# Kernel tuning notes

Hardware: AMD Instinct MI355X
Metric: run time of the kernel (lower is better)

Reference implementation:

```python
import jax, jax.numpy as jnp
import numpy as np

MUL = 256            # multiplicity of each irrep block
S = MUL              # scalar (0e) block width
V = MUL * 3          # vector (1e) block width
D = S + V            # total feature width = 1024
N = 32768            # number of nodes
INV3 = 1.0 / np.sqrt(3.0)   # w3j(1,1,0) and w3j(0,1,1) coefficient
INV6 = 1.0 / np.sqrt(6.0)   # w3j(1,1,1) (Levi-Civita) coefficient
A0 = np.sqrt(1.0 / 5.0)     # path weight for 0e outputs: sqrt(dim_out / n_paths) = sqrt(1/5)
A1 = np.sqrt(3.0 / 5.0)     # path weight for 1e outputs: sqrt(3/5)


def _split(x):
    # x: [N, D] -> scalars [N, MUL], vectors [N, MUL, 3]
    return x[:, :S], x[:, S:].reshape(x.shape[0], MUL, 3)


def norm_gate(x, w1, b1, w2, b2):
    # NormGate: gates = MLP([scalars, |vectors|]); out = [gates_s, vectors * gates_v]
    s, v = _split(x)
    nv = jnp.sqrt(jnp.sum(v * v, axis=-1) + 1e-12)           # [N, MUL] per-irrep norms
    f0 = jnp.concatenate([s, nv], axis=-1)                    # [N, 2*MUL]
    g = jax.nn.silu(f0 @ w1 + b1) @ w2 + b2                   # [N, 2*MUL]
    gated = v * g[:, S:, None]                                # ElementwiseTensorProduct with 0e gates
    return jnp.concatenate([g[:, :S], gated.reshape(-1, V)], axis=-1)


def irrep_linear(x, w0, b0, w1):
    # e3nn o3.Linear: per-l multiplicity mixing with 1/sqrt(fan_in) normalization; bias only on 0e
    s, v = _split(x)
    so = s @ (w0 / np.sqrt(MUL)) + b0
    vo = jnp.einsum('nui,uw->nwi', v, w1 / np.sqrt(MUL))
    return jnp.concatenate([so, vo.reshape(-1, V)], axis=-1)


def tensor_product(x1, x2, w):
    # 'uuu' CG tensor product, 5 instructions: (0,0)->0, (0,1)->1, (1,0)->1, (1,1)->0, (1,1)->1
    # w: [5, MUL] per-path per-u learned weights
    s1, v1 = _split(x1)
    s2, v2 = _split(x2)
    out0 = A0 * (w[0] * s1 * s2 + w[3] * INV3 * jnp.sum(v1 * v2, axis=-1))   # [N, MUL]
    out1 = A1 * (INV3 * (w[1] * s1)[:, :, None] * v2
                 + INV3 * (w[2] * s2)[:, :, None] * v1
                 + INV6 * w[4][None, :, None] * jnp.cross(v1, v2))           # [N, MUL, 3]
    return jnp.concatenate([out0, out1.reshape(-1, V)], axis=-1)


def setup_inputs() -> dict:
    key = jax.random.key(0)
    ks = jax.random.split(key, 32)
    d = {}
    d['x'] = jax.random.normal(ks[0], (N, D), dtype=jnp.float32)
    d['old_fii'] = jax.random.normal(ks[1], (N, D), dtype=jnp.float32)
    i = 2
    for pre in ('ng1', 'ng2', 'ngo'):
        d[pre + '_w1'] = jax.random.normal(ks[i], (2 * MUL, 2 * MUL), dtype=jnp.float32) / np.sqrt(2 * MUL); i += 1
        d[pre + '_b1'] = jax.random.normal(ks[i], (2 * MUL,), dtype=jnp.float32) * 0.01; i += 1
        d[pre + '_w2'] = jax.random.normal(ks[i], (2 * MUL, 2 * MUL), dtype=jnp.float32) / np.sqrt(2 * MUL); i += 1
        d[pre + '_b2'] = jax.random.normal(ks[i], (2 * MUL,), dtype=jnp.float32) * 0.01; i += 1
    for pre in ('lin1', 'lin2', 'lin3'):
        d[pre + '_w0'] = jax.random.normal(ks[i], (MUL, MUL), dtype=jnp.float32); i += 1
        d[pre + '_b0'] = jax.random.normal(ks[i], (MUL,), dtype=jnp.float32) * 0.01; i += 1
        d[pre + '_w1'] = jax.random.normal(ks[i], (MUL, MUL), dtype=jnp.float32); i += 1
    d['tp_w'] = jax.random.normal(ks[i], (5, MUL), dtype=jnp.float32)
    return d


def reference(x, old_fii,
              ng1_w1, ng1_b1, ng1_w2, ng1_b2,
              ng2_w1, ng2_b1, ng2_w2, ng2_b2,
              ngo_w1, ngo_b1, ngo_w2, ngo_b2,
              lin1_w0, lin1_b0, lin1_w1,
              lin2_w0, lin2_b0, lin2_w1,
              lin3_w0, lin3_b0, lin3_w1,
              tp_w):
    xl = irrep_linear(norm_gate(x, ng1_w1, ng1_b1, ng1_w2, ng1_b2), lin1_w0, lin1_b0, lin1_w1)
    xr = irrep_linear(norm_gate(x, ng2_w1, ng2_b1, ng2_w2, ng2_b2), lin2_w0, lin2_b0, lin2_w1)
    t = tensor_product(xl, xr, tp_w) + x        # resnet (dims match)
    t = irrep_linear(norm_gate(t, ngo_w1, ngo_b1, ngo_w2, ngo_b2), lin3_w0, lin3_b0, lin3_w1)
    return old_fii + t
```

## Files before the change

kernel.cpp:

```cpp
#include <hip/hip_runtime.h>
#include <stdint.h>
#include <math.h>

typedef unsigned short u16;
typedef __attribute__((ext_vector_type(8))) short short8;
typedef __attribute__((ext_vector_type(4))) float f32x4;

#define A0C 0.44721359549995793f
#define A1C 0.77459666924148340f
#define INV3C 0.57735026918962584f
#define INV6C 0.40824829046386302f

__device__ __forceinline__ float bf2f(u16 u) {
    unsigned v = ((unsigned)u) << 16; float f; __builtin_memcpy(&f, &v, 4); return f;
}
__device__ __forceinline__ u16 f2bf(float f) {
    unsigned u; __builtin_memcpy(&u, &f, 4);
    u += 0x7fffu + ((u >> 16) & 1u);
    return (u16)(u >> 16);
}

__device__ __forceinline__ void gload_lds16(const void* g, void* l) {
    __builtin_amdgcn_global_load_lds((const __attribute__((address_space(1))) unsigned*)g,
                                     (__attribute__((address_space(3))) unsigned*)l, 16, 0, 0);
}

union S8 { short8 v; u16 h[8]; };

struct WDesc { const float* s; u16* d; int n; float sc; };
struct WArgs { WDesc w[12]; };

__global__ void cvt_weights(WArgs args) {
    WDesc wd = args.w[blockIdx.z];
    int n = wd.n;
    int x0 = blockIdx.x * 32, y0 = blockIdx.y * 32;
    if (x0 >= n || y0 >= n) return;
    __shared__ float tile[32][33];
    int tx = threadIdx.x, ty = threadIdx.y;
#pragma unroll
    for (int j = 0; j < 4; j++)
        tile[ty + 8 * j][tx] = wd.s[(size_t)(y0 + ty + 8 * j) * n + x0 + tx];
    __syncthreads();
#pragma unroll
    for (int j = 0; j < 4; j++)
        wd.d[(size_t)(x0 + ty + 8 * j) * n + y0 + tx] = f2bf(tile[tx][ty + 8 * j] * wd.sc);
}

struct BDesc { const float* s; float* d; int n; };
struct BArgs { BDesc b[9]; };
__global__ void pack_bias(BArgs a) {
    BDesc b = a.b[blockIdx.x];
    for (int i = threadIdx.x; i < b.n; i += 256) b.d[i] = b.s[i];
}

__global__ void prep_f0(const float* __restrict__ x, u16* __restrict__ f0,
                        u16* __restrict__ xv, long ps) {
    int t = blockIdx.x * 256 + threadIdx.x;
    long n = t >> 5;
    int u0 = (t & 31) * 8;
    const float* xr = x + (size_t)n * 1024;
    float4 s0 = *(const float4*)(xr + u0);
    float4 s1 = *(const float4*)(xr + u0 + 4);
    float vv[24];
#pragma unroll
    for (int i = 0; i < 6; i++) {
        float4 w = *(const float4*)(xr + 256 + 3 * u0 + 4 * i);
        vv[4 * i] = w.x; vv[4 * i + 1] = w.y; vv[4 * i + 2] = w.z; vv[4 * i + 3] = w.w;
    }
    float sc[8] = { s0.x, s0.y, s0.z, s0.w, s1.x, s1.y, s1.z, s1.w };
    S8 fs, fn, px, py, pz;
#pragma unroll
    for (int j = 0; j < 8; j++) {
        float a = vv[3 * j], b = vv[3 * j + 1], c = vv[3 * j + 2];
        float nv = sqrtf(a * a + b * b + c * c + 1e-12f);
        fs.h[j] = f2bf(sc[j]);
        fn.h[j] = f2bf(nv);
        px.h[j] = f2bf(a); py.h[j] = f2bf(b); pz.h[j] = f2bf(c);
    }
    size_t o = (size_t)n * 256 + u0;
    *(short8*)(f0 + (size_t)n * 512 + u0) = fs.v;
    *(short8*)(f0 + (size_t)n * 512 + 256 + u0) = fn.v;
    *(short8*)(xv + o) = px.v;
    *(short8*)(xv + ps + o) = py.v;
    *(short8*)(xv + 2 * ps + o) = pz.v;
}

__global__ __launch_bounds__(512, 2)
void gemm256(const u16* __restrict__ Ap, int lda, long az,
             const u16* __restrict__ xsrc,
             const u16* __restrict__ gp, int gld, long gz,
             const u16* __restrict__ Bt, long bz, long bw,
             const float* __restrict__ bias, int bsz,
             u16* __restrict__ C, int ldc, long czs, long czp,
             int K, long nc, int mode, int act, int nshift)
{
    extern __shared__ __align__(16) u16 sm[];
    u16* As = sm;
    u16* Bs = sm + 32768;

    const int tid = threadIdx.x;
    const int lane = tid & 63;
    const int wid = tid >> 6;
    const int wr = wid >> 2, wc = wid & 3;
    const int lr = lane & 15, hk = lane >> 4;

    int nwg = gridDim.x;
    int lid = blockIdx.x;
    int wg;
    if ((nwg & 7) == 0) { int q = nwg >> 3; wg = (lid & 7) * q + (lid >> 3); }
    else wg = lid;
    const long row0 = (long)(wg >> nshift) * 256;
    const int n0 = (wg & ((1 << nshift) - 1)) * 256;
    const int zi = blockIdx.y;

    long p = 0, rr0 = row0;
    if (mode == 2) { p = row0 / nc; rr0 = row0 - p * nc; }

    const u16* Bz = Bt + (size_t)zi * bz + ((mode == 2 && p > 0) ? bw : 0);
    const long cbase = (mode == 2) ? (zi * czs + p * czp + rr0 * ldc)
                                   : (zi * czs + row0 * ldc);

    f32x4 acc[8][4];
#pragma unroll
    for (int m = 0; m < 8; m++)
#pragma unroll
        for (int n = 0; n < 4; n++) acc[m][n] = (f32x4){0.f, 0.f, 0.f, 0.f};

    auto stageB = [&](int buf, int kt) {
#pragma unroll
        for (int it = 0; it < 4; ++it) {
            int idx = it * 512 + tid;
            int r = idx >> 3, s = idx & 7;
            const u16* g = Bz + (size_t)(n0 + r) * K + kt + ((s ^ (r & 7)) * 8);
            u16* l = Bs + buf * 16384 + (size_t)(it * 512 + (tid & 0x1C0)) * 8;
            gload_lds16(g, l);
        }
    };
    auto stageA0 = [&](int buf, int kt) {
#pragma unroll
        for (int it = 0; it < 4; ++it) {
            int idx = it * 512 + tid;
            int r = idx >> 3, s = idx & 7;
            const u16* g = Ap + (size_t)zi * az + (rr0 + r) * (size_t)lda + kt + ((s ^ (r & 7)) * 8);
            u16* l = As + buf * 16384 + (size_t)(it * 512 + (tid & 0x1C0)) * 8;
            gload_lds16(g, l);
        }
    };
    auto stageA2 = [&](int buf, int kt) {
#pragma unroll
        for (int it = 0; it < 4; ++it) {
            int idx = it * 512 + tid;
            int r = idx >> 3, s = idx & 7;
            int u = kt + s * 8;
            S8 gg, tu, pk;
            gg.v = *(const short8*)(gp + (size_t)zi * gz + (rr0 + r) * (size_t)gld + 256 + u);
            tu.v = *(const short8*)(xsrc + (size_t)(row0 - nc + r) * 256 + u);
#pragma unroll
            for (int j = 0; j < 8; j++) pk.h[j] = f2bf(bf2f(tu.h[j]) * bf2f(gg.h[j]));
            *(short8*)&As[buf * 16384 + ((size_t)r * 8 + (s ^ (r & 7))) * 8] = pk.v;
        }
    };

    const bool a_direct = (mode == 0) || (p == 0);
    const int nt = K >> 6;
    stageB(0, 0);
    if (a_direct) stageA0(0, 0); else stageA2(0, 0);
    __syncthreads();

    int buf = 0;
    for (int t = 0; t < nt; ++t) {
        if (t + 1 < nt) {
            int kt = (t + 1) << 6;
            stageB(buf ^ 1, kt);
            if (a_direct) stageA0(buf ^ 1, kt); else stageA2(buf ^ 1, kt);
        }
        const int ao = buf * 16384, bo = buf * 16384;
#pragma unroll
        for (int kk = 0; kk < 2; ++kk) {
            short8 b[4];
#pragma unroll
            for (int n = 0; n < 4; n++) {
                int cb = wc * 64 + n * 16 + lr;
                int sl = (kk * 4 + hk) ^ (cb & 7);
                b[n] = *(const short8*)&Bs[bo + (size_t)cb * 64 + sl * 8];
            }
#pragma unroll
            for (int m = 0; m < 8; m++) {
                int ra = wr * 128 + m * 16 + lr;
                int sl = (kk * 4 + hk) ^ (ra & 7);
                short8 a = *(const short8*)&As[ao + (size_t)ra * 64 + sl * 8];
#pragma unroll
                for (int n = 0; n < 4; n++)
                    acc[m][n] = __builtin_amdgcn_mfma_f32_16x16x32_bf16(b[n], a, acc[m][n], 0, 0, 0);
            }
        }
        __syncthreads();
        buf ^= 1;
    }

    const bool use_bias = bias && (mode == 0 || p == 0);
#pragma unroll
    for (int m = 0; m < 8; m++) {
        long rit = wr * 128 + m * 16 + lr;
        u16* crow = C + cbase + rit * (size_t)ldc;
#pragma unroll
        for (int n = 0; n < 4; n++) {
            int col = n0 + wc * 64 + n * 16 + hk * 4;
            float4 bb = use_bias ? *(const float4*)&bias[(size_t)zi * bsz + col]
                                 : (float4){0.f, 0.f, 0.f, 0.f};
            float v0 = acc[m][n][0] + bb.x;
            float v1 = acc[m][n][1] + bb.y;
            float v2 = acc[m][n][2] + bb.z;
            float v3 = acc[m][n][3] + bb.w;
            if (act) {
                v0 = v0 * (1.0f / (1.0f + __expf(-v0)));
                v1 = v1 * (1.0f / (1.0f + __expf(-v1)));
                v2 = v2 * (1.0f / (1.0f + __expf(-v2)));
                v3 = v3 * (1.0f / (1.0f + __expf(-v3)));
            }
            uint2 st;
            st.x = (unsigned)f2bf(v0) | ((unsigned)f2bf(v1) << 16);
            st.y = (unsigned)f2bf(v2) | ((unsigned)f2bf(v3) << 16);
            *(uint2*)(crow + col) = st;
        }
    }
}

__global__ void tp_res(const u16* __restrict__ xl, const u16* xr_,
                       const float* __restrict__ tpw, const u16* __restrict__ xv,
                       u16* f0, u16* tv, long ps)
{
    int t = blockIdx.x * 256 + threadIdx.x;
    long n = t >> 5;
    int u0 = (t & 31) * 8;
    size_t o = (size_t)n * 256 + u0;

    S8 S1, AX, AY, AZ, S2, BX, BY, BZ, XS, RX, RY, RZ;
    S1.v = *(const short8*)(xl + o);
    AX.v = *(const short8*)(xl + ps + o);
    AY.v = *(const short8*)(xl + 2 * ps + o);
    AZ.v = *(const short8*)(xl + 3 * ps + o);
    S2.v = *(const short8*)(xr_ + o);
    BX.v = *(const short8*)(xr_ + ps + o);
    BY.v = *(const short8*)(xr_ + 2 * ps + o);
    BZ.v = *(const short8*)(xr_ + 3 * ps + o);
    XS.v = *(const short8*)(f0 + (size_t)n * 512 + u0);
    RX.v = *(const short8*)(xv + o);
    RY.v = *(const short8*)(xv + ps + o);
    RZ.v = *(const short8*)(xv + 2 * ps + o);

    float W[5][8];
#pragma unroll
    for (int q = 0; q < 5; q++) {
        float4 a = *(const float4*)(tpw + q * 256 + u0);
        float4 b = *(const float4*)(tpw + q * 256 + u0 + 4);
        W[q][0] = a.x; W[q][1] = a.y; W[q][2] = a.z; W[q][3] = a.w;
        W[q][4] = b.x; W[q][5] = b.y; W[q][6] = b.z; W[q][7] = b.w;
    }

    S8 O0, NV, TX, TY, TZ;
#pragma unroll
    for (int j = 0; j < 8; j++) {
        float s1 = bf2f(S1.h[j]), a1x = bf2f(AX.h[j]), a1y = bf2f(AY.h[j]), a1z = bf2f(AZ.h[j]);
        float s2 = bf2f(S2.h[j]), b1x = bf2f(BX.h[j]), b1y = bf2f(BY.h[j]), b1z = bf2f(BZ.h[j]);
        float dot = a1x * b1x + a1y * b1y + a1z * b1z;
        float cx = a1y * b1z - a1z * b1y;
        float cy = a1z * b1x - a1x * b1z;
        float cz = a1x * b1y - a1y * b1x;
        float out0 = A0C * (W[0][j] * s1 * s2 + W[3][j] * INV3C * dot) + bf2f(XS.h[j]);
        float ox = A1C * (INV3C * (W[1][j] * s1 * b1x + W[2][j] * s2 * a1x) + INV6C * W[4][j] * cx) + bf2f(RX.h[j]);
        float oy = A1C * (INV3C * (W[1][j] * s1 * b1y + W[2][j] * s2 * a1y) + INV6C * W[4][j] * cy) + bf2f(RY.h[j]);
        float oz = A1C * (INV3C * (W[1][j] * s1 * b1z + W[2][j] * s2 * a1z) + INV6C * W[4][j] * cz) + bf2f(RZ.h[j]);
        float nv = sqrtf(ox * ox + oy * oy + oz * oz + 1e-12f);
        O0.h[j] = f2bf(out0);
        NV.h[j] = f2bf(nv);
        TX.h[j] = f2bf(ox); TY.h[j] = f2bf(oy); TZ.h[j] = f2bf(oz);
    }
    *(short8*)(f0 + (size_t)n * 512 + u0) = O0.v;
    *(short8*)(f0 + (size_t)n * 512 + 256 + u0) = NV.v;
    *(short8*)(tv + o) = TX.v;
    *(short8*)(tv + ps + o) = TY.v;
    *(short8*)(tv + 2 * ps + o) = TZ.v;
}

__global__ void repack(const u16* __restrict__ outp, const float* __restrict__ old,
                       float* __restrict__ out, long ps)
{
    int t = blockIdx.x * 256 + threadIdx.x;
    long n = t >> 5;
    int u0 = (t & 31) * 8;
    size_t o = (size_t)n * 256 + u0;

    S8 S, VX, VY, VZ;
    S.v  = *(const short8*)(outp + o);
    VX.v = *(const short8*)(outp + ps + o);
    VY.v = *(const short8*)(outp + 2 * ps + o);
    VZ.v = *(const short8*)(outp + 3 * ps + o);

    const float* oldr = old + (size_t)n * 1024;
    float* outr = out + (size_t)n * 1024;

#pragma unroll
    for (int i = 0; i < 2; i++) {
        float4 ov = *(const float4*)(oldr + u0 + 4 * i);
        float4 r;
        r.x = ov.x + bf2f(S.h[4 * i]);
        r.y = ov.y + bf2f(S.h[4 * i + 1]);
        r.z = ov.z + bf2f(S.h[4 * i + 2]);
        r.w = ov.w + bf2f(S.h[4 * i + 3]);
        *(float4*)(outr + u0 + 4 * i) = r;
    }
    float vv[24];
#pragma unroll
    for (int j = 0; j < 8; j++) {
        vv[3 * j] = bf2f(VX.h[j]);
        vv[3 * j + 1] = bf2f(VY.h[j]);
        vv[3 * j + 2] = bf2f(VZ.h[j]);
    }
#pragma unroll
    for (int i = 0; i < 6; i++) {
        float4 ov = *(const float4*)(oldr + 256 + 3 * u0 + 4 * i);
        float4 r;
        r.x = ov.x + vv[4 * i];
        r.y = ov.y + vv[4 * i + 1];
        r.z = ov.z + vv[4 * i + 2];
        r.w = ov.w + vv[4 * i + 3];
        *(float4*)(outr + 256 + 3 * u0 + 4 * i) = r;
    }
}

enum {
    OFF_ng12w1 = 0,
    OFF_ng1w2  = 524288,
    OFF_ngow1  = 1048576,
    OFF_ngow2  = 1310720,
    OFF_l12w0  = 1572864,
    OFF_l12w1  = 1703936,
    OFF_l3w0   = 1835008,
    OFF_l3w1   = 1900544
};
#define BIAS_BYTE_OFF 3932160
enum { BOFF_mlp1 = 0, BOFF_mlp2 = 1024, BOFF_ngo1 = 2048, BOFF_ngo2 = 2560,
       BOFF_l12 = 3072, BOFF_l3 = 3584 };

extern "C" void kernel_launch(void* const* d_in, const int* in_sizes, int n_in,
                              void* d_out, int out_size, void* d_ws, size_t ws_size,
                              hipStream_t stream) {
    const float* x      = (const float*)d_in[0];
    const float* oldf   = (const float*)d_in[1];
    const float* ng1_w1 = (const float*)d_in[2];
    const float* ng1_b1 = (const float*)d_in[3];
    const float* ng1_w2 = (const float*)d_in[4];
    const float* ng1_b2 = (const float*)d_in[5];
    const float* ng2_w1 = (const float*)d_in[6];
    const float* ng2_b1 = (const float*)d_in[7];
    const float* ng2_w2 = (const float*)d_in[8];
    const float* ng2_b2 = (const float*)d_in[9];
    const float* ngo_w1 = (const float*)d_in[10];
    const float* ngo_b1 = (const float*)d_in[11];
    const float* ngo_w2 = (const float*)d_in[12];
    const float* ngo_b2 = (const float*)d_in[13];
    const float* l1_w0  = (const float*)d_in[14];
    const float* l1_b0  = (const float*)d_in[15];
    const float* l1_w1  = (const float*)d_in[16];
    const float* l2_w0  = (const float*)d_in[17];
    const float* l2_b0  = (const float*)d_in[18];
    const float* l2_w1  = (const float*)d_in[19];
    const float* l3_w0  = (const float*)d_in[20];
    const float* l3_b0  = (const float*)d_in[21];
    const float* l3_w1  = (const float*)d_in[22];
    const float* tpw    = (const float*)d_in[23];

    u16* wts = (u16*)d_ws;
    char* wsb = (char*)d_ws;
    float* biasf = (float*)(wsb + BIAS_BYTE_OFF);

    WArgs wa;
    wa.w[0]  = { ng1_w1, wts + OFF_ng12w1,          512, 1.0f };
    wa.w[1]  = { ng2_w1, wts + OFF_ng12w1 + 262144, 512, 1.0f };
    wa.w[2]  = { ng1_w2, wts + OFF_ng1w2,           512, 1.0f };
    wa.w[3]  = { ng2_w2, wts + OFF_ng1w2 + 262144,  512, 1.0f };
    wa.w[4]  = { ngo_w1, wts + OFF_ngow1,           512, 1.0f };
    wa.w[5]  = { ngo_w2, wts + OFF_ngow2,           512, 1.0f };
    wa.w[6]  = { l1_w0, wts + OFF_l12w0,            256, 0.0625f };
    wa.w[7]  = { l2_w0, wts + OFF_l12w0 + 65536,    256, 0.0625f };
    wa.w[8]  = { l1_w1, wts + OFF_l12w1,            256, 0.0625f };
    wa.w[9]  = { l2_w1, wts + OFF_l12w1 + 65536,    256, 0.0625f };
    wa.w[10] = { l3_w0, wts + OFF_l3w0,             256, 0.0625f };
    wa.w[11] = { l3_w1, wts + OFF_l3w1,             256, 0.0625f };
    cvt_weights<<<dim3(16, 16, 12), dim3(32, 8), 0, stream>>>(wa);

    BArgs ba;
    ba.b[0] = { ng1_b1, biasf + BOFF_mlp1,       512 };
    ba.b[1] = { ng2_b1, biasf + BOFF_mlp1 + 512, 512 };
    ba.b[2] = { ng1_b2, biasf + BOFF_mlp2,       512 };
    ba.b[3] = { ng2_b2, biasf + BOFF_mlp2 + 512, 512 };
    ba.b[4] = { ngo_b1, biasf + BOFF_ngo1,       512 };
    ba.b[5] = { ngo_b2, biasf + BOFF_ngo2,       512 };
    ba.b[6] = { l1_b0, biasf + BOFF_l12,         256 };
    ba.b[7] = { l2_b0, biasf + BOFF_l12 + 256,   256 };
    ba.b[8] = { l3_b0, biasf + BOFF_l3,          256 };
    pack_bias<<<9, 256, 0, stream>>>(ba);

    long Nn = (long)in_sizes[0] / 1024;

    int c = 1;
    while (c < 256 &&
           (unsigned long long)(4ULL << 20) + (unsigned long long)(Nn / c) * 10752ULL > (unsigned long long)ws_size)
        c <<= 1;
    long Nc = Nn / c;

    u16* F0 = (u16*)(wsb + (4 << 20));
    u16* H  = F0 + (size_t)Nc * 512;
    u16* G  = H + (size_t)Nc * 1024;
    u16* XV = G + (size_t)Nc * 1024;
    u16* XL = XV + (size_t)Nc * 768;
    long ps = Nc * 256;
    u16* XR = XL + 4 * ps;
    u16* TV = XR + ps;
    u16* OUTP = XL;

    dim3 blk(512);
    const size_t SMEM = 131072;
    int mt = (int)(Nc / 256);
    int eb = (int)(Nc / 8);

    for (int ch = 0; ch < c; ++ch) {
        const float* xk  = x + (size_t)ch * Nc * 1024;
        const float* ok  = oldf + (size_t)ch * Nc * 1024;
        float* outk = (float*)d_out + (size_t)ch * Nc * 1024;

        prep_f0<<<eb, 256, 0, stream>>>(xk, F0, XV, ps);

        gemm256<<<dim3(mt * 4, 1), blk, SMEM, stream>>>(F0, 512, 0, nullptr, nullptr, 0, 0,
            wts + OFF_ng12w1, 0, 0, biasf + BOFF_mlp1, 0, H, 1024, 0, 0, 512, Nc, 0, 1, 2);
        gemm256<<<dim3(mt * 2, 2), blk, SMEM, stream>>>(H, 1024, 512, nullptr, nullptr, 0, 0,
            wts + OFF_ng1w2, 262144, 0, biasf + BOFF_mlp2, 512, G, 1024, 512, 0, 512, Nc, 0, 0, 1);
        gemm256<<<dim3(mt * 4, 2), blk, SMEM, stream>>>(G, 1024, 512, XV, G, 1024, 512,
            wts + OFF_l12w0, 65536, 131072, biasf + BOFF_l12, 256, XL, 256, 4 * ps, ps, 256, Nc, 2, 0, 0);

        tp_res<<<eb, 256, 0, stream>>>(XL, XR, tpw, XV, F0, TV, ps);

        gemm256<<<dim3(mt * 2, 1), blk, SMEM, stream>>>(F0, 512, 0, nullptr, nullptr, 0, 0,
            wts + OFF_ngow1, 0, 0, biasf + BOFF_ngo1, 0, H, 512, 0, 0, 512, Nc, 0, 1, 1);
        gemm256<<<dim3(mt * 2, 1), blk, SMEM, stream>>>(H, 512, 0, nullptr, nullptr, 0, 0,
            wts + OFF_ngow2, 0, 0, biasf + BOFF_ngo2, 0, G, 512, 0, 0, 512, Nc, 0, 0, 1);
        gemm256<<<dim3(mt * 4, 1), blk, SMEM, stream>>>(G, 512, 0, TV, G, 512, 0,
            wts + OFF_l3w0, 0, 65536, biasf + BOFF_l3, 0, OUTP, 256, 0, ps, 256, Nc, 2, 0, 0);

        repack<<<eb, 256, 0, stream>>>(OUTP, ok, outk, ps);
    }
}
```

Measured before the change: 504.3 us.

## Shrink GEMM tiles to 128x128 with single-buffered static LDS

Replaces the 256x256-tile, 512-thread, double-buffered GEMM with a 128x128-tile, 256-thread kernel that uses 32 KB of static shared memory and a single buffer. Each k-step loads, syncs, computes and syncs again. The smaller tile and footprint should let more workgroups fit per CU and give better load balance across the grid. In exchange it gives up the overlap between global loads and MFMA work, and each loaded element is reused less.

```diff
diff --git a/kernel.cpp b/kernel.cpp
--- a/kernel.cpp
+++ b/kernel.cpp
@@ -85,8 +85,8 @@
     *(short8*)(xv + 2 * ps + o) = pz.v;
 }
 
-__global__ __launch_bounds__(512, 2)
-void gemm256(const u16* __restrict__ Ap, int lda, long az,
+__global__ __launch_bounds__(256, 4)
+void gemm128(const u16* __restrict__ Ap, int lda, long az,
              const u16* __restrict__ xsrc,
              const u16* __restrict__ gp, int gld, long gz,
              const u16* __restrict__ Bt, long bz, long bw,
@@ -94,14 +94,13 @@
              u16* __restrict__ C, int ldc, long czs, long czp,
              int K, long nc, int mode, int act, int nshift)
 {
-    extern __shared__ __align__(16) u16 sm[];
-    u16* As = sm;
-    u16* Bs = sm + 32768;
+    __shared__ __align__(16) u16 As[128 * 64];
+    __shared__ __align__(16) u16 Bs[128 * 64];
 
     const int tid = threadIdx.x;
     const int lane = tid & 63;
     const int wid = tid >> 6;
-    const int wr = wid >> 2, wc = wid & 3;
+    const int wr = wid >> 1, wc = wid & 1;
     const int lr = lane & 15, hk = lane >> 4;
 
     int nwg = gridDim.x;
@@ -109,8 +108,8 @@
     int wg;
     if ((nwg & 7) == 0) { int q = nwg >> 3; wg = (lid & 7) * q + (lid >> 3); }
     else wg = lid;
-    const long row0 = (long)(wg >> nshift) * 256;
-    const int n0 = (wg & ((1 << nshift) - 1)) * 256;
+    const long row0 = (long)(wg >> nshift) * 128;
+    const int n0 = (wg & ((1 << nshift) - 1)) * 128;
     const int zi = blockIdx.y;
 
     long p = 0, rr0 = row0;
@@ -120,61 +119,48 @@
     const long cbase = (mode == 2) ? (zi * czs + p * czp + rr0 * ldc)
                                    : (zi * czs + row0 * ldc);
 
-    f32x4 acc[8][4];
-#pragma unroll
-    for (int m = 0; m < 8; m++)
+    f32x4 acc[4][4];
+#pragma unroll
+    for (int m = 0; m < 4; m++)
 #pragma unroll
         for (int n = 0; n < 4; n++) acc[m][n] = (f32x4){0.f, 0.f, 0.f, 0.f};
-
-    auto stageB = [&](int buf, int kt) {
-#pragma unroll
-        for (int it = 0; it < 4; ++it) {
-            int idx = it * 512 + tid;
-            int r = idx >> 3, s = idx & 7;
-            const u16* g = Bz + (size_t)(n0 + r) * K + kt + ((s ^ (r & 7)) * 8);
-            u16* l = Bs + buf * 16384 + (size_t)(it * 512 + (tid & 0x1C0)) * 8;
-            gload_lds16(g, l);
-        }
-    };
-    auto stageA0 = [&](int buf, int kt) {
-#pragma unroll
-        for (int it = 0; it < 4; ++it) {
-            int idx = it * 512 + tid;
-            int r = idx >> 3, s = idx & 7;
-            const u16* g = Ap + (size_t)zi * az + (rr0 + r) * (size_t)lda + kt + ((s ^ (r & 7)) * 8);
-            u16* l = As + buf * 16384 + (size_t)(it * 512 + (tid & 0x1C0)) * 8;
-            gload_lds16(g, l);
-        }
-    };
-    auto stageA2 = [&](int buf, int kt) {
-#pragma unroll
-        for (int it = 0; it < 4; ++it) {
-            int idx = it * 512 + tid;
-            int r = idx >> 3, s = idx & 7;
-            int u = kt + s * 8;
-            S8 gg, tu, pk;
-            gg.v = *(const short8*)(gp + (size_t)zi * gz + (rr0 + r) * (size_t)gld + 256 + u);
-            tu.v = *(const short8*)(xsrc + (size_t)(row0 - nc + r) * 256 + u);
-#pragma unroll
-            for (int j = 0; j < 8; j++) pk.h[j] = f2bf(bf2f(tu.h[j]) * bf2f(gg.h[j]));
-            *(short8*)&As[buf * 16384 + ((size_t)r * 8 + (s ^ (r & 7))) * 8] = pk.v;
-        }
-    };
 
     const bool a_direct = (mode == 0) || (p == 0);
     const int nt = K >> 6;
-    stageB(0, 0);
-    if (a_direct) stageA0(0, 0); else stageA2(0, 0);
-    __syncthreads();
-
-    int buf = 0;
+
     for (int t = 0; t < nt; ++t) {
-        if (t + 1 < nt) {
-            int kt = (t + 1) << 6;
-            stageB(buf ^ 1, kt);
-            if (a_direct) stageA0(buf ^ 1, kt); else stageA2(buf ^ 1, kt);
+        const int kt = t << 6;
+#pragma unroll
+        for (int it = 0; it < 4; ++it) {
+            int idx = it * 256 + tid;
+            int r = idx >> 3, s = idx & 7;
+            gload_lds16(Bz + (size_t)(n0 + r) * K + kt + ((s ^ (r & 7)) * 8),
+                        &Bs[(size_t)(it * 256 + (tid & 192)) * 8]);
         }
-        const int ao = buf * 16384, bo = buf * 16384;
+        if (a_direct) {
+#pragma unroll
+            for (int it = 0; it < 4; ++it) {
+                int idx = it * 256 + tid;
+                int r = idx >> 3, s = idx & 7;
+                gload_lds16(Ap + (size_t)zi * az + (rr0 + r) * (size_t)lda + kt + ((s ^ (r & 7)) * 8),
+                            &As[(size_t)(it * 256 + (tid & 192)) * 8]);
+            }
+        } else {
+#pragma unroll
+            for (int it = 0; it < 4; ++it) {
+                int idx = it * 256 + tid;
+                int r = idx >> 3, s = idx & 7;
+                int u = kt + s * 8;
+                S8 gg, tu, pk;
+                gg.v = *(const short8*)(gp + (size_t)zi * gz + (rr0 + r) * (size_t)gld + 256 + u);
+                tu.v = *(const short8*)(xsrc + (size_t)(row0 - nc + r) * 256 + u);
+#pragma unroll
+                for (int j = 0; j < 8; j++) pk.h[j] = f2bf(bf2f(tu.h[j]) * bf2f(gg.h[j]));
+                *(short8*)&As[((size_t)r * 8 + (s ^ (r & 7))) * 8] = pk.v;
+            }
+        }
+        __syncthreads();
+
 #pragma unroll
         for (int kk = 0; kk < 2; ++kk) {
             short8 b[4];
@@ -182,26 +168,25 @@
             for (int n = 0; n < 4; n++) {
                 int cb = wc * 64 + n * 16 + lr;
                 int sl = (kk * 4 + hk) ^ (cb & 7);
-                b[n] = *(const short8*)&Bs[bo + (size_t)cb * 64 + sl * 8];
+                b[n] = *(const short8*)&Bs[(size_t)cb * 64 + sl * 8];
             }
 #pragma unroll
-            for (int m = 0; m < 8; m++) {
-                int ra = wr * 128 + m * 16 + lr;
+            for (int m = 0; m < 4; m++) {
+                int ra = wr * 64 + m * 16 + lr;
                 int sl = (kk * 4 + hk) ^ (ra & 7);
-                short8 a = *(const short8*)&As[ao + (size_t)ra * 64 + sl * 8];
+                short8 a = *(const short8*)&As[(size_t)ra * 64 + sl * 8];
 #pragma unroll
                 for (int n = 0; n < 4; n++)
                     acc[m][n] = __builtin_amdgcn_mfma_f32_16x16x32_bf16(b[n], a, acc[m][n], 0, 0, 0);
             }
         }
         __syncthreads();
-        buf ^= 1;
     }
 
     const bool use_bias = bias && (mode == 0 || p == 0);
 #pragma unroll
-    for (int m = 0; m < 8; m++) {
-        long rit = wr * 128 + m * 16 + lr;
+    for (int m = 0; m < 4; m++) {
+        long rit = wr * 64 + m * 16 + lr;
         u16* crow = C + cbase + rit * (size_t)ldc;
 #pragma unroll
         for (int n = 0; n < 4; n++) {
@@ -420,9 +405,8 @@
     u16* TV = XR + ps;
     u16* OUTP = XL;
 
-    dim3 blk(512);
-    const size_t SMEM = 131072;
-    int mt = (int)(Nc / 256);
+    dim3 blk(256);
+    int mt = (int)(Nc / 128);
     int eb = (int)(Nc / 8);
 
     for (int ch = 0; ch < c; ++ch) {
@@ -432,21 +416,21 @@
 
         prep_f0<<<eb, 256, 0, stream>>>(xk, F0, XV, ps);
 
-        gemm256<<<dim3(mt * 4, 1), blk, SMEM, stream>>>(F0, 512, 0, nullptr, nullptr, 0, 0,
-            wts + OFF_ng12w1, 0, 0, biasf + BOFF_mlp1, 0, H, 1024, 0, 0, 512, Nc, 0, 1, 2);
-        gemm256<<<dim3(mt * 2, 2), blk, SMEM, stream>>>(H, 1024, 512, nullptr, nullptr, 0, 0,
-            wts + OFF_ng1w2, 262144, 0, biasf + BOFF_mlp2, 512, G, 1024, 512, 0, 512, Nc, 0, 0, 1);
-        gemm256<<<dim3(mt * 4, 2), blk, SMEM, stream>>>(G, 1024, 512, XV, G, 1024, 512,
-            wts + OFF_l12w0, 65536, 131072, biasf + BOFF_l12, 256, XL, 256, 4 * ps, ps, 256, Nc, 2, 0, 0);
+        gemm128<<<dim3(mt * 8, 1), blk, 0, stream>>>(F0, 512, 0, nullptr, nullptr, 0, 0,
+            wts + OFF_ng12w1, 0, 0, biasf + BOFF_mlp1, 0, H, 1024, 0, 0, 512, Nc, 0, 1, 3);
+        gemm128<<<dim3(mt * 4, 2), blk, 0, stream>>>(H, 1024, 512, nullptr, nullptr, 0, 0,
+            wts + OFF_ng1w2, 262144, 0, biasf + BOFF_mlp2, 512, G, 1024, 512, 0, 512, Nc, 0, 0, 2);
+        gemm128<<<dim3(mt * 8, 2), blk, 0, stream>>>(G, 1024, 512, XV, G, 1024, 512,
+            wts + OFF_l12w0, 65536, 131072, biasf + BOFF_l12, 256, XL, 256, 4 * ps, ps, 256, Nc, 2, 0, 1);
 
         tp_res<<<eb, 256, 0, stream>>>(XL, XR, tpw, XV, F0, TV, ps);
 
-        gemm256<<<dim3(mt * 2, 1), blk, SMEM, stream>>>(F0, 512, 0, nullptr, nullptr, 0, 0,
-            wts + OFF_ngow1, 0, 0, biasf + BOFF_ngo1, 0, H, 512, 0, 0, 512, Nc, 0, 1, 1);
-        gemm256<<<dim3(mt * 2, 1), blk, SMEM, stream>>>(H, 512, 0, nullptr, nullptr, 0, 0,
-            wts + OFF_ngow2, 0, 0, biasf + BOFF_ngo2, 0, G, 512, 0, 0, 512, Nc, 0, 0, 1);
-        gemm256<<<dim3(mt * 4, 1), blk, SMEM, stream>>>(G, 512, 0, TV, G, 512, 0,
-            wts + OFF_l3w0, 0, 65536, biasf + BOFF_l3, 0, OUTP, 256, 0, ps, 256, Nc, 2, 0, 0);
+        gemm128<<<dim3(mt * 4, 1), blk, 0, stream>>>(F0, 512, 0, nullptr, nullptr, 0, 0,
+            wts + OFF_ngow1, 0, 0, biasf + BOFF_ngo1, 0, H, 512, 0, 0, 512, Nc, 0, 1, 2);
+        gemm128<<<dim3(mt * 4, 1), blk, 0, stream>>>(H, 512, 0, nullptr, nullptr, 0, 0,
+            wts + OFF_ngow2, 0, 0, biasf + BOFF_ngo2, 0, G, 512, 0, 0, 512, Nc, 0, 0, 2);
+        gemm128<<<dim3(mt * 8, 1), blk, 0, stream>>>(G, 512, 0, TV, G, 512, 0,
+            wts + OFF_l3w0, 0, 65536, biasf + BOFF_l3, 0, OUTP, 256, 0, ps, 256, Nc, 2, 0, 1);
 
         repack<<<eb, 256, 0, stream>>>(OUTP, ok, outk, ps);
     }
```

After: 537.3 us. 1.07x slower.
